# Optimization experiments

Hardware: AMD Instinct MI355X
Metric: run time of the kernel (lower is better)

Reference implementation:

```python
import jax, jax.numpy as jnp
import numpy as np

N_NODES = 100000
N_EDGES = 1600000
IN_CH = 128          # 127 node features + 1 node_attr
HIDDEN = 2           # hidd_FV_size
OUT_CH = 128
ATTR = 6


def setup_inputs() -> dict:
    key = jax.random.key(0)
    ks = jax.random.split(key, 8)
    x = jax.random.normal(ks[0], (N_NODES, IN_CH - 1), dtype=jnp.float32)
    node_attr = jax.random.normal(ks[1], (N_NODES, 1), dtype=jnp.float32)
    edge_index = jax.random.randint(ks[2], (2, N_EDGES), 0, N_NODES, dtype=jnp.int64)
    edge_attr = jax.random.normal(ks[3], (N_EDGES, ATTR), dtype=jnp.float32)
    # lin_in: Linear(ATTR, HIDDEN * IN_CH); lin_out: Linear(HIDDEN * IN_CH, OUT_CH)
    W_in = jax.random.normal(ks[4], (ATTR, HIDDEN * IN_CH), dtype=jnp.float32) / np.sqrt(ATTR)
    b_in = jax.random.normal(ks[5], (HIDDEN * IN_CH,), dtype=jnp.float32) * 0.01
    W_out = jax.random.normal(ks[6], (HIDDEN * IN_CH, OUT_CH), dtype=jnp.float32) / np.sqrt(HIDDEN * IN_CH)
    b_out = jax.random.normal(ks[7], (OUT_CH,), dtype=jnp.float32) * 0.01
    return {"x": x, "node_attr": node_attr, "edge_index": edge_index,
            "edge_attr": edge_attr, "W_in": W_in, "b_in": b_in,
            "W_out": W_out, "b_out": b_out}


def reference(x, node_attr, edge_index, edge_attr, W_in, b_in, W_out, b_out):
    # forward: x = cat(x, node_attr) -> propagate(aggr='add') -> update
    xc = jnp.concatenate([x, node_attr], axis=1)                # [N, IN_CH]
    src, dst = edge_index[0], edge_index[1]                     # PyG: message from x_j=src, aggregated at dst
    x_j = xc[src]                                               # [E, IN_CH] gather
    # message: scaling = relu(lin_in(edge_attr)); result = scaling.reshape(E,C,H) * x_j[...,None]
    scaling = jax.nn.relu(edge_attr @ W_in + b_in)              # [E, C*H]
    msg = (scaling.reshape(-1, IN_CH, HIDDEN) * x_j[:, :, None]).reshape(-1, IN_CH * HIDDEN)
    # aggregate: scatter-add over destination nodes
    aggr = jax.ops.segment_sum(msg, dst, num_segments=N_NODES)  # [N, C*H]
    # update: lin_out -> tanh (dropout p=0 / eval mode)
    return jnp.tanh(aggr @ W_out + b_out)                       # [N, OUT_CH]
```

## Files before the change

### kernel.cpp

```cpp
#include <hip/hip_runtime.h>


#define ATTR 6
#define SCAN_CHUNK 1024


__global__ __launch_bounds__(256) void hist_kernel(
    const int* __restrict__ ei, int* __restrict__ counts, int E)
{
  const int e0 = blockIdx.x * 1024 + threadIdx.x * 4;
  if (((E & 3) == 0) && (e0 + 4 <= E)) {
    const int4 d = *(const int4*)(ei + E + e0);
    atomicAdd(&counts[d.x], 1);
    atomicAdd(&counts[d.y], 1);
    atomicAdd(&counts[d.z], 1);
    atomicAdd(&counts[d.w], 1);
  } else {
#pragma unroll
    for (int j = 0; j < 4; ++j) {
      const int e = e0 + j;
      if (e < E) atomicAdd(&counts[ei[E + e]], 1);
    }
  }
}


__global__ __launch_bounds__(256) void scan1_kernel(
    const int* __restrict__ counts, int* __restrict__ offsets,
    int* __restrict__ bsum, int N)
{
  __shared__ int sdata[256];
  const int t = threadIdx.x;
  const int base = blockIdx.x * SCAN_CHUNK + t * 4;
  int c[4]; int s = 0;
#pragma unroll
  for (int j = 0; j < 4; ++j) { int i = base + j; c[j] = (i < N) ? counts[i] : 0; s += c[j]; }
  sdata[t] = s;
  __syncthreads();
  for (int d = 1; d < 256; d <<= 1) {
    int tv = (t >= d) ? sdata[t - d] : 0;
    __syncthreads();
    sdata[t] += tv;
    __syncthreads();
  }
  int excl = sdata[t] - s;
#pragma unroll
  for (int j = 0; j < 4; ++j) { int i = base + j; if (i < N) offsets[i] = excl; excl += c[j]; }
  if (t == 255) bsum[blockIdx.x] = sdata[255];
}


__global__ __launch_bounds__(256) void scanB_kernel(
    int* __restrict__ offsets, int* __restrict__ cursors,
    const int* __restrict__ bsum, int N, int E)
{
  __shared__ int red[4];
  const int t = threadIdx.x;
  int v = 0;
  for (int k = t; k < (int)blockIdx.x; k += 256) v += bsum[k];
#pragma unroll
  for (int d = 32; d > 0; d >>= 1) v += __shfl_down(v, d, 64);
  if ((t & 63) == 0) red[t >> 6] = v;
  __syncthreads();
  const int add = red[0] + red[1] + red[2] + red[3];

  const int base = blockIdx.x * SCAN_CHUNK + t * 4;
#pragma unroll
  for (int j = 0; j < 4; ++j) {
    const int i = base + j;
    if (i < N) { const int o = offsets[i] + add; offsets[i] = o; cursors[i] = o; }
  }
  if (blockIdx.x == 0 && t == 0) offsets[N] = E;
}


__global__ __launch_bounds__(256) void scatter_concat_kernel(
    const int* __restrict__ ei, const float* __restrict__ ea,
    int* __restrict__ cursors, int* __restrict__ srcs, float* __restrict__ eas,
    const float* __restrict__ x, const float* __restrict__ na,
    float* __restrict__ xc, int E, int N, int SB)
{
  if ((int)blockIdx.x < SB) {
    const int e = blockIdx.x * 256 + threadIdx.x;
    if (e < E) {
      const int dst = ei[E + e];
      const int slot = atomicAdd(&cursors[dst], 1);
      srcs[slot] = ei[e];
      const float2 a0 = *(const float2*)(ea + (size_t)e * ATTR + 0);
      const float2 a1 = *(const float2*)(ea + (size_t)e * ATTR + 2);
      const float2 a2 = *(const float2*)(ea + (size_t)e * ATTR + 4);
      float* ep = eas + (size_t)slot * ATTR;
      *(float2*)(ep + 0) = a0;
      *(float2*)(ep + 2) = a1;
      *(float2*)(ep + 4) = a2;
    }
  } else {
    const int gid = (blockIdx.x - SB) * 256 + threadIdx.x;
    const int row = gid >> 5;
    const int c4 = (gid & 31) * 4;
    if (row < N) {
      const float* xr = x + (size_t)row * 127;
      float4 v;
      v.x = xr[c4];
      v.y = xr[c4 + 1];
      v.z = xr[c4 + 2];
      v.w = (c4 == 124) ? na[row] : xr[c4 + 3];
      *(float4*)(xc + (size_t)row * 128 + c4) = v;
    }
  }
}


__global__ __launch_bounds__(256) void aggregate8b_kernel(
    const float* __restrict__ xc,
    const float* __restrict__ W_in, const float* __restrict__ b_in,
    const int* __restrict__ offsets, const int* __restrict__ srcs,
    const float* __restrict__ eas,
    float* __restrict__ aggr, int N)
{
  const int L = threadIdx.x & 63;
  const int n = __builtin_amdgcn_readfirstlane(blockIdx.x * 4 + (threadIdx.x >> 6));
  if (n >= N) return;

  float2 wlo[ATTR], whi[ATTR];
#pragma unroll
  for (int a = 0; a < ATTR; ++a) {
    wlo[a] = *(const float2*)(W_in + a * 256 + 2 * L);
    whi[a] = *(const float2*)(W_in + a * 256 + 128 + 2 * L);
  }
  const float2 blo = *(const float2*)(b_in + 2 * L);
  const float2 bhi = *(const float2*)(b_in + 128 + 2 * L);

  float alo0 = 0.f, alo1 = 0.f, ahi0 = 0.f, ahi1 = 0.f;
  const int beg = __builtin_amdgcn_readfirstlane(offsets[n]);
  const int end = __builtin_amdgcn_readfirstlane(offsets[n + 1]);

  int i0 = beg;
  for (; i0 + 8 <= end; i0 += 8) {
    int s8[8];
#pragma unroll
    for (int j = 0; j < 8; ++j) s8[j] = srcs[i0 + j];
    float eav[8][ATTR];
#pragma unroll
    for (int j = 0; j < 8; ++j)
#pragma unroll
      for (int a = 0; a < ATTR; ++a) eav[j][a] = eas[(size_t)(i0 + j) * ATTR + a];

    float xlo[8], xhi[8];
#pragma unroll
    for (int j = 0; j < 8; ++j) {
      const float* xr = xc + (size_t)s8[j] * 128;
      xlo[j] = xr[L];
      xhi[j] = xr[64 + L];
    }
#pragma unroll
    for (int j = 0; j < 8; ++j) {
      float sl0 = blo.x, sl1 = blo.y, sh0 = bhi.x, sh1 = bhi.y;
#pragma unroll
      for (int a = 0; a < ATTR; ++a) {
        sl0 = fmaf(eav[j][a], wlo[a].x, sl0);
        sl1 = fmaf(eav[j][a], wlo[a].y, sl1);
        sh0 = fmaf(eav[j][a], whi[a].x, sh0);
        sh1 = fmaf(eav[j][a], whi[a].y, sh1);
      }
      sl0 = fmaxf(sl0, 0.f); sl1 = fmaxf(sl1, 0.f);
      sh0 = fmaxf(sh0, 0.f); sh1 = fmaxf(sh1, 0.f);
      alo0 = fmaf(sl0, xlo[j], alo0);
      alo1 = fmaf(sl1, xlo[j], alo1);
      ahi0 = fmaf(sh0, xhi[j], ahi0);
      ahi1 = fmaf(sh1, xhi[j], ahi1);
    }
  }
  if (i0 + 4 <= end) {
    int s4[4];
#pragma unroll
    for (int j = 0; j < 4; ++j) s4[j] = srcs[i0 + j];
    float eav[4][ATTR];
#pragma unroll
    for (int j = 0; j < 4; ++j)
#pragma unroll
      for (int a = 0; a < ATTR; ++a) eav[j][a] = eas[(size_t)(i0 + j) * ATTR + a];
    float xlo[4], xhi[4];
#pragma unroll
    for (int j = 0; j < 4; ++j) {
      const float* xr = xc + (size_t)s4[j] * 128;
      xlo[j] = xr[L];
      xhi[j] = xr[64 + L];
    }
#pragma unroll
    for (int j = 0; j < 4; ++j) {
      float sl0 = blo.x, sl1 = blo.y, sh0 = bhi.x, sh1 = bhi.y;
#pragma unroll
      for (int a = 0; a < ATTR; ++a) {
        sl0 = fmaf(eav[j][a], wlo[a].x, sl0);
        sl1 = fmaf(eav[j][a], wlo[a].y, sl1);
        sh0 = fmaf(eav[j][a], whi[a].x, sh0);
        sh1 = fmaf(eav[j][a], whi[a].y, sh1);
      }
      sl0 = fmaxf(sl0, 0.f); sl1 = fmaxf(sl1, 0.f);
      sh0 = fmaxf(sh0, 0.f); sh1 = fmaxf(sh1, 0.f);
      alo0 = fmaf(sl0, xlo[j], alo0);
      alo1 = fmaf(sl1, xlo[j], alo1);
      ahi0 = fmaf(sh0, xhi[j], ahi0);
      ahi1 = fmaf(sh1, xhi[j], ahi1);
    }
    i0 += 4;
  }
  for (; i0 < end; ++i0) {
    const int s = srcs[i0];
    float eav[ATTR];
#pragma unroll
    for (int a = 0; a < ATTR; ++a) eav[a] = eas[(size_t)i0 * ATTR + a];
    const float* xr = xc + (size_t)s * 128;
    const float xl = xr[L];
    const float xh = xr[64 + L];
    float sl0 = blo.x, sl1 = blo.y, sh0 = bhi.x, sh1 = bhi.y;
#pragma unroll
    for (int a = 0; a < ATTR; ++a) {
      sl0 = fmaf(eav[a], wlo[a].x, sl0);
      sl1 = fmaf(eav[a], wlo[a].y, sl1);
      sh0 = fmaf(eav[a], whi[a].x, sh0);
      sh1 = fmaf(eav[a], whi[a].y, sh1);
    }
    sl0 = fmaxf(sl0, 0.f); sl1 = fmaxf(sl1, 0.f);
    sh0 = fmaxf(sh0, 0.f); sh1 = fmaxf(sh1, 0.f);
    alo0 = fmaf(sl0, xl, alo0);
    alo1 = fmaf(sl1, xl, alo1);
    ahi0 = fmaf(sh0, xh, ahi0);
    ahi1 = fmaf(sh1, xh, ahi1);
  }

  *(float2*)(aggr + (size_t)n * 256 + 2 * L)       = make_float2(alo0, alo1);
  *(float2*)(aggr + (size_t)n * 256 + 128 + 2 * L) = make_float2(ahi0, ahi1);
}


__global__ __launch_bounds__(256) void scatter_kernel(
    const int* __restrict__ ei, int* __restrict__ cursors,
    int* __restrict__ perm, int* __restrict__ srcs, int E)
{
  int e = blockIdx.x * 256 + threadIdx.x;
  if (e < E) {
    int dst = ei[E + e];
    int slot = atomicAdd(&cursors[dst], 1);
    perm[slot] = e;
    srcs[slot] = ei[e];
  }
}

__global__ __launch_bounds__(256) void aggregate4_kernel(
    const float* __restrict__ x, const float* __restrict__ node_attr,
    const int* __restrict__ ei, const float* __restrict__ ea,
    const float* __restrict__ W_in, const float* __restrict__ b_in,
    const int* __restrict__ offsets, const int* __restrict__ perm,
    const int* __restrict__ srcs,
    float* __restrict__ aggr, int N)
{
  const int L = threadIdx.x & 63;
  const int n = __builtin_amdgcn_readfirstlane(blockIdx.x * 4 + (threadIdx.x >> 6));
  if (n >= N) return;

  float2 wlo[ATTR], whi[ATTR];
#pragma unroll
  for (int a = 0; a < ATTR; ++a) {
    wlo[a] = *(const float2*)(W_in + a * 256 + 2 * L);
    whi[a] = *(const float2*)(W_in + a * 256 + 128 + 2 * L);
  }
  const float2 blo = *(const float2*)(b_in + 2 * L);
  const float2 bhi = *(const float2*)(b_in + 128 + 2 * L);

  float alo0 = 0.f, alo1 = 0.f, ahi0 = 0.f, ahi1 = 0.f;
  const int beg = offsets[n], end = offsets[n + 1];

  for (int i0 = beg; i0 < end; i0 += 4) {
    const int cnt = end - i0;
    int e4[4], s4[4];
#pragma unroll
    for (int j = 0; j < 4; ++j) {
      const int idx = i0 + ((j < cnt) ? j : cnt - 1);
      e4[j] = perm[idx];
      s4[j] = srcs[idx];
    }
    float eav[4][ATTR];
#pragma unroll
    for (int j = 0; j < 4; ++j)
#pragma unroll
      for (int a = 0; a < ATTR; ++a) eav[j][a] = ea[(size_t)e4[j] * ATTR + a];
    float xlo[4], xhi[4];
#pragma unroll
    for (int j = 0; j < 4; ++j) {
      const float* xr = x + (size_t)s4[j] * 127;
      xlo[j] = xr[L];
      xhi[j] = (L == 63) ? node_attr[s4[j]] : xr[64 + L];
    }
#pragma unroll
    for (int j = 0; j < 4; ++j)
      if (j >= cnt) { xlo[j] = 0.f; xhi[j] = 0.f; }
#pragma unroll
    for (int j = 0; j < 4; ++j) {
      float sl0 = blo.x, sl1 = blo.y, sh0 = bhi.x, sh1 = bhi.y;
#pragma unroll
      for (int a = 0; a < ATTR; ++a) {
        sl0 = fmaf(eav[j][a], wlo[a].x, sl0);
        sl1 = fmaf(eav[j][a], wlo[a].y, sl1);
        sh0 = fmaf(eav[j][a], whi[a].x, sh0);
        sh1 = fmaf(eav[j][a], whi[a].y, sh1);
      }
      sl0 = fmaxf(sl0, 0.f); sl1 = fmaxf(sl1, 0.f);
      sh0 = fmaxf(sh0, 0.f); sh1 = fmaxf(sh1, 0.f);
      alo0 = fmaf(sl0, xlo[j], alo0);
      alo1 = fmaf(sl1, xlo[j], alo1);
      ahi0 = fmaf(sh0, xhi[j], ahi0);
      ahi1 = fmaf(sh1, xhi[j], ahi1);
    }
  }

  *(float2*)(aggr + (size_t)n * 256 + 2 * L)       = make_float2(alo0, alo1);
  *(float2*)(aggr + (size_t)n * 256 + 128 + 2 * L) = make_float2(ahi0, ahi1);
}


__global__ __launch_bounds__(256) void edge_kernel(
    const float* __restrict__ x, const float* __restrict__ node_attr,
    const int* __restrict__ ei, const float* __restrict__ ea,
    const float* __restrict__ W_in, const float* __restrict__ b_in,
    float* __restrict__ aggr, int E, int N, int epw)
{
  const int lane = threadIdx.x & 63;
  const int wave = blockIdx.x * (blockDim.x >> 6) + (threadIdx.x >> 6);
  const int k0 = lane << 2;
  const int c0 = lane << 1;

  float w[ATTR][4];
#pragma unroll
  for (int a = 0; a < ATTR; ++a) {
    const float4 t = *(const float4*)(W_in + a * 256 + k0);
    w[a][0] = t.x; w[a][1] = t.y; w[a][2] = t.z; w[a][3] = t.w;
  }
  const float4 bt = *(const float4*)(b_in + k0);

  const long e0 = (long)wave * epw;
  for (int i = 0; i < epw; ++i) {
    const long e = e0 + i;
    if (e >= E) return;
    const int src = ei[e];
    const int dst = ei[E + e];

    float eav[ATTR];
#pragma unroll
    for (int a = 0; a < ATTR; ++a) eav[a] = ea[(size_t)e * ATTR + a];

    float s0 = bt.x, s1 = bt.y, s2 = bt.z, s3 = bt.w;
#pragma unroll
    for (int a = 0; a < ATTR; ++a) {
      s0 = fmaf(eav[a], w[a][0], s0);
      s1 = fmaf(eav[a], w[a][1], s1);
      s2 = fmaf(eav[a], w[a][2], s2);
      s3 = fmaf(eav[a], w[a][3], s3);
    }
    s0 = fmaxf(s0, 0.f); s1 = fmaxf(s1, 0.f);
    s2 = fmaxf(s2, 0.f); s3 = fmaxf(s3, 0.f);

    const float* xr = x + (size_t)src * 127;
    const float x0 = xr[c0];
    const float x1 = (lane == 63) ? node_attr[src] : xr[c0 + 1];

    float* ap = aggr + (size_t)dst * 256 + k0;
    atomicAdd(ap + 0, s0 * x0);
    atomicAdd(ap + 1, s1 * x0);
    atomicAdd(ap + 2, s2 * x1);
    atomicAdd(ap + 3, s3 * x1);
  }
}


__global__ __launch_bounds__(256) void node_kernel2(
    const float* __restrict__ aggr, const float* __restrict__ W_out,
    const float* __restrict__ b_out, float* __restrict__ out, int N)
{
  __shared__ float Wl[64 * 128];
  __shared__ float Al[64][68];
  const int t = threadIdx.x;
  const int o4 = (t & 31) * 4;
  const int ng = t >> 5;
  const int nbase = blockIdx.x * 64;

  float acc[8][4];
#pragma unroll
  for (int j = 0; j < 8; ++j)
#pragma unroll
    for (int q = 0; q < 4; ++q) acc[j][q] = 0.f;

  for (int kc = 0; kc < 4; ++kc) {
    __syncthreads();
    const float4* wsrc = (const float4*)(W_out + kc * 64 * 128);
    float4* wdst = (float4*)Wl;
#pragma unroll
    for (int i = 0; i < 8; ++i) wdst[t + 256 * i] = wsrc[t + 256 * i];
    {
      const int r = t >> 2, q = t & 3;
      int row = nbase + r; if (row >= N) row = N - 1;
      const float4* asrc = (const float4*)(aggr + (size_t)row * 256 + kc * 64 + q * 16);
      float4 v0 = asrc[0], v1 = asrc[1], v2 = asrc[2], v3 = asrc[3];
      float4* adst = (float4*)&Al[r][q * 16];
      adst[0] = v0; adst[1] = v1; adst[2] = v2; adst[3] = v3;
    }
    __syncthreads();

    for (int k = 0; k < 64; k += 4) {
      float4 a4[8];
#pragma unroll
      for (int j = 0; j < 8; ++j) a4[j] = *(const float4*)&Al[ng * 8 + j][k];
#pragma unroll
      for (int kk = 0; kk < 4; ++kk) {
        const float4 w4 = *(const float4*)&Wl[(k + kk) * 128 + o4];
#pragma unroll
        for (int j = 0; j < 8; ++j) {
          const float av = (&a4[j].x)[kk];
          acc[j][0] = fmaf(av, w4.x, acc[j][0]);
          acc[j][1] = fmaf(av, w4.y, acc[j][1]);
          acc[j][2] = fmaf(av, w4.z, acc[j][2]);
          acc[j][3] = fmaf(av, w4.w, acc[j][3]);
        }
      }
    }
  }

  const float4 b4 = *(const float4*)(b_out + o4);
#pragma unroll
  for (int j = 0; j < 8; ++j) {
    const int n = nbase + ng * 8 + j;
    if (n < N) {
      float4 r;
      r.x = tanhf(acc[j][0] + b4.x);
      r.y = tanhf(acc[j][1] + b4.y);
      r.z = tanhf(acc[j][2] + b4.z);
      r.w = tanhf(acc[j][3] + b4.w);
      *(float4*)(out + (size_t)n * 128 + o4) = r;
    }
  }
}


extern "C" void kernel_launch(void* const* d_in, const int* in_sizes, int n_in,
                              void* d_out, int out_size, void* d_ws, size_t ws_size,
                              hipStream_t stream) {
  const float* x         = (const float*)d_in[0];
  const float* node_attr = (const float*)d_in[1];
  const int*   ei        = (const int*)d_in[2];
  const float* ea        = (const float*)d_in[3];
  const float* W_in      = (const float*)d_in[4];
  const float* b_in      = (const float*)d_in[5];
  const float* W_out     = (const float*)d_in[6];
  const float* b_out     = (const float*)d_in[7];
  float* out = (float*)d_out;

  const int N = in_sizes[0] / 127;
  const int E = in_sizes[2] / 2;

  auto align16 = [](size_t v) { return (v + 15) & ~(size_t)15; };
  const size_t szCounts  = align16((size_t)N * 4);
  const size_t szOffsets = align16(((size_t)N + 1) * 4);
  const size_t szCursors = align16((size_t)N * 4);
  const size_t szBsum    = align16(((size_t)N / SCAN_CHUNK + 2) * 4);
  const size_t szPerm    = align16((size_t)E * 4);
  const size_t szSrcs    = align16((size_t)E * 4);
  const size_t szEas     = align16((size_t)E * ATTR * 4);
  const size_t szXc      = align16((size_t)N * 128 * 4);
  const size_t szAggr    = (size_t)N * 256 * 4;

  const size_t needA = szCounts + szOffsets + szCursors + szBsum +
                       szSrcs + szEas + szXc + szAggr;
  const size_t needB = szCounts + szOffsets + szCursors + szBsum +
                       szPerm + szSrcs + szAggr;

  const int nodeBlocks = (N + 63) / 64;
  const int histBlocks = (E + 1023) / 1024;
  const int nb = (N + SCAN_CHUNK - 1) / SCAN_CHUNK;
  const int SB = (E + 255) / 256;
  const int CB = (N * 32 + 255) / 256;

  if (ws_size >= needA) {
    char* p = (char*)d_ws;
    int* counts   = (int*)p;     p += szCounts;
    int* offsets  = (int*)p;     p += szOffsets;
    int* cursors  = (int*)p;     p += szCursors;
    int* bsum     = (int*)p;     p += szBsum;
    int* srcs     = (int*)p;     p += szSrcs;
    float* eas    = (float*)p;   p += szEas;
    float* xc     = (float*)p;   p += szXc;
    float* aggr   = (float*)p;

    hipMemsetAsync(counts, 0, szCounts, stream);
    hist_kernel<<<histBlocks, 256, 0, stream>>>(ei, counts, E);
    scan1_kernel<<<nb, 256, 0, stream>>>(counts, offsets, bsum, N);
    scanB_kernel<<<nb, 256, 0, stream>>>(offsets, cursors, bsum, N, E);
    scatter_concat_kernel<<<SB + CB, 256, 0, stream>>>(
        ei, ea, cursors, srcs, eas, x, node_attr, xc, E, N, SB);
    aggregate8b_kernel<<<(N + 3) / 4, 256, 0, stream>>>(
        xc, W_in, b_in, offsets, srcs, eas, aggr, N);
    node_kernel2<<<nodeBlocks, 256, 0, stream>>>(aggr, W_out, b_out, out, N);
  } else if (ws_size >= needB) {
    char* p = (char*)d_ws;
    int* counts   = (int*)p;     p += szCounts;
    int* offsets  = (int*)p;     p += szOffsets;
    int* cursors  = (int*)p;     p += szCursors;
    int* bsum     = (int*)p;     p += szBsum;
    int* perm     = (int*)p;     p += szPerm;
    int* srcs     = (int*)p;     p += szSrcs;
    float* aggr   = (float*)p;

    hipMemsetAsync(counts, 0, szCounts, stream);
    hist_kernel<<<histBlocks, 256, 0, stream>>>(ei, counts, E);
    scan1_kernel<<<nb, 256, 0, stream>>>(counts, offsets, bsum, N);
    scanB_kernel<<<nb, 256, 0, stream>>>(offsets, cursors, bsum, N, E);
    scatter_kernel<<<SB, 256, 0, stream>>>(ei, cursors, perm, srcs, E);
    aggregate4_kernel<<<(N + 3) / 4, 256, 0, stream>>>(
        x, node_attr, ei, ea, W_in, b_in, offsets, perm, srcs, aggr, N);
    node_kernel2<<<nodeBlocks, 256, 0, stream>>>(aggr, W_out, b_out, out, N);
  } else {
    float* aggr = (float*)d_ws;
    hipMemsetAsync(aggr, 0, (size_t)N * 256 * 4, stream);
    const int EPW = 4;
    const int waves = (E + EPW - 1) / EPW;
    edge_kernel<<<(waves + 3) / 4, 256, 0, stream>>>(
        x, node_attr, ei, ea, W_in, b_in, aggr, E, N, EPW);
    node_kernel2<<<nodeBlocks, 256, 0, stream>>>(aggr, W_out, b_out, out, N);
  }
}
```

Before: 565.4 us.

## Pack CSR edge payload into 32-byte records and use packed float2 FMA

The scatter stage now writes the source index and six edge attributes into one 32-byte record per sorted slot, instead of separate srcs and eas arrays. The new aggregation kernel reads each record as two float4 loads, gathers a float2 per lane from the concatenated node features, and computes scaling and accumulation with float2 FMA helpers that could map to packed FP32 instructions. The output GEMM kernel is also rewritten with float2 accumulators, and 64-bit index math is replaced with 32-bit. The packed layout uses a little more workspace because of the padding slot, and 32-bit indexing limits the maximum problem size.

```diff
diff --git a/kernel.cpp b/kernel.cpp
--- a/kernel.cpp
+++ b/kernel.cpp
@@ -3,6 +3,15 @@
 
 #define ATTR 6
 #define SCAN_CHUNK 1024
+
+
+__device__ __forceinline__ float2 f2fma(float2 a, float2 b, float2 c) {
+  return make_float2(fmaf(a.x, b.x, c.x), fmaf(a.y, b.y, c.y));
+}
+__device__ __forceinline__ float2 f2max0(float2 a) {
+  return make_float2(fmaxf(a.x, 0.f), fmaxf(a.y, 0.f));
+}
+__device__ __forceinline__ float2 f2splat(float x) { return make_float2(x, x); }
 
 
 __global__ __launch_bounds__(256) void hist_kernel(
@@ -71,6 +80,111 @@
     if (i < N) { const int o = offsets[i] + add; offsets[i] = o; cursors[i] = o; }
   }
   if (blockIdx.x == 0 && t == 0) offsets[N] = E;
+}
+
+
+__global__ __launch_bounds__(256) void scatter_concat2_kernel(
+    const int* __restrict__ ei, const float* __restrict__ ea,
+    int* __restrict__ cursors, float* __restrict__ pay,
+    const float* __restrict__ x, const float* __restrict__ na,
+    float* __restrict__ xc, int E, int N, int SB)
+{
+  if ((int)blockIdx.x < SB) {
+    const int e = blockIdx.x * 256 + threadIdx.x;
+    if (e < E) {
+      const int dst = ei[E + e];
+      const int slot = atomicAdd(&cursors[dst], 1);
+      const float2 a0 = *(const float2*)(ea + e * ATTR + 0);
+      const float2 a1 = *(const float2*)(ea + e * ATTR + 2);
+      const float2 a2 = *(const float2*)(ea + e * ATTR + 4);
+      float4* pp = (float4*)pay + 2 * slot;
+      pp[0] = make_float4(__int_as_float(ei[e]), a0.x, a0.y, a1.x);
+      pp[1] = make_float4(a1.y, a2.x, a2.y, 0.f);
+    }
+  } else {
+    const int gid = (blockIdx.x - SB) * 256 + threadIdx.x;
+    const int row = gid >> 5;
+    const int c4 = (gid & 31) * 4;
+    if (row < N) {
+      const float* xr = x + row * 127;
+      float4 v;
+      v.x = xr[c4];
+      v.y = xr[c4 + 1];
+      v.z = xr[c4 + 2];
+      v.w = (c4 == 124) ? na[row] : xr[c4 + 3];
+      *(float4*)(xc + row * 128 + c4) = v;
+    }
+  }
+}
+
+
+template <int G>
+__device__ __forceinline__ void agg_group(
+    const float4* pp, const float* xc, int L,
+    const float2* wA, const float2* wB, float2 bA, float2 bB,
+    float2& accA, float2& accB)
+{
+  float4 p0[G], p1[G];
+#pragma unroll
+  for (int j = 0; j < G; ++j) { p0[j] = pp[2 * j]; p1[j] = pp[2 * j + 1]; }
+  float2 xv[G];
+#pragma unroll
+  for (int j = 0; j < G; ++j) {
+    const int s = __float_as_int(p0[j].x);
+    xv[j] = *(const float2*)(xc + s * 128 + 2 * L);
+  }
+#pragma unroll
+  for (int j = 0; j < G; ++j) {
+    float2 sA = bA, sB = bB;
+    sA = f2fma(f2splat(p0[j].y), wA[0], sA); sB = f2fma(f2splat(p0[j].y), wB[0], sB);
+    sA = f2fma(f2splat(p0[j].z), wA[1], sA); sB = f2fma(f2splat(p0[j].z), wB[1], sB);
+    sA = f2fma(f2splat(p0[j].w), wA[2], sA); sB = f2fma(f2splat(p0[j].w), wB[2], sB);
+    sA = f2fma(f2splat(p1[j].x), wA[3], sA); sB = f2fma(f2splat(p1[j].x), wB[3], sB);
+    sA = f2fma(f2splat(p1[j].y), wA[4], sA); sB = f2fma(f2splat(p1[j].y), wB[4], sB);
+    sA = f2fma(f2splat(p1[j].z), wA[5], sA); sB = f2fma(f2splat(p1[j].z), wB[5], sB);
+    sA = f2max0(sA); sB = f2max0(sB);
+    accA = f2fma(f2splat(xv[j].x), sA, accA);
+    accB = f2fma(f2splat(xv[j].y), sB, accB);
+  }
+}
+
+__global__ __launch_bounds__(256) void aggregate_v3_kernel(
+    const float* __restrict__ xc,
+    const float* __restrict__ W_in, const float* __restrict__ b_in,
+    const int* __restrict__ offsets, const float* __restrict__ pay,
+    float* __restrict__ aggr, int N)
+{
+  const int L = (int)threadIdx.x & 63;
+  const int n = __builtin_amdgcn_readfirstlane((int)blockIdx.x * 4 + ((int)threadIdx.x >> 6));
+  if (n >= N) return;
+
+  float2 wA[ATTR], wB[ATTR];
+#pragma unroll
+  for (int a = 0; a < ATTR; ++a) {
+    const float4 w4 = *(const float4*)(W_in + a * 256 + 4 * L);
+    wA[a] = make_float2(w4.x, w4.y);
+    wB[a] = make_float2(w4.z, w4.w);
+  }
+  const float4 b4 = *(const float4*)(b_in + 4 * L);
+  const float2 bA = make_float2(b4.x, b4.y);
+  const float2 bB = make_float2(b4.z, b4.w);
+
+  float2 accA = make_float2(0.f, 0.f);
+  float2 accB = make_float2(0.f, 0.f);
+  const int beg = __builtin_amdgcn_readfirstlane(offsets[n]);
+  const int end = __builtin_amdgcn_readfirstlane(offsets[n + 1]);
+
+  int i0 = beg;
+  for (; i0 + 8 <= end; i0 += 8)
+    agg_group<8>((const float4*)pay + 2 * i0, xc, L, wA, wB, bA, bB, accA, accB);
+  if (i0 + 4 <= end) {
+    agg_group<4>((const float4*)pay + 2 * i0, xc, L, wA, wB, bA, bB, accA, accB);
+    i0 += 4;
+  }
+  for (; i0 < end; ++i0)
+    agg_group<1>((const float4*)pay + 2 * i0, xc, L, wA, wB, bA, bB, accA, accB);
+
+  *(float4*)(aggr + n * 256 + 4 * L) = make_float4(accA.x, accA.y, accB.x, accB.y);
 }
 
 
@@ -110,7 +224,6 @@
   }
 }
 
-
 __global__ __launch_bounds__(256) void aggregate8b_kernel(
     const float* __restrict__ xc,
     const float* __restrict__ W_in, const float* __restrict__ b_in,
@@ -374,7 +487,7 @@
 }
 
 
-__global__ __launch_bounds__(256) void node_kernel2(
+__global__ __launch_bounds__(256) void node_kernel3(
     const float* __restrict__ aggr, const float* __restrict__ W_out,
     const float* __restrict__ b_out, float* __restrict__ out, int N)
 {
@@ -385,11 +498,12 @@
   const int ng = t >> 5;
   const int nbase = blockIdx.x * 64;
 
-  float acc[8][4];
-#pragma unroll
-  for (int j = 0; j < 8; ++j)
-#pragma unroll
-    for (int q = 0; q < 4; ++q) acc[j][q] = 0.f;
+  float2 acc[8][2];
+#pragma unroll
+  for (int j = 0; j < 8; ++j) {
+    acc[j][0] = make_float2(0.f, 0.f);
+    acc[j][1] = make_float2(0.f, 0.f);
+  }
 
   for (int kc = 0; kc < 4; ++kc) {
     __syncthreads();
@@ -400,7 +514,7 @@
     {
       const int r = t >> 2, q = t & 3;
       int row = nbase + r; if (row >= N) row = N - 1;
-      const float4* asrc = (const float4*)(aggr + (size_t)row * 256 + kc * 64 + q * 16);
+      const float4* asrc = (const float4*)(aggr + row * 256 + kc * 64 + q * 16);
       float4 v0 = asrc[0], v1 = asrc[1], v2 = asrc[2], v3 = asrc[3];
       float4* adst = (float4*)&Al[r][q * 16];
       adst[0] = v0; adst[1] = v1; adst[2] = v2; adst[3] = v3;
@@ -414,13 +528,13 @@
 #pragma unroll
       for (int kk = 0; kk < 4; ++kk) {
         const float4 w4 = *(const float4*)&Wl[(k + kk) * 128 + o4];
+        const float2 wA = make_float2(w4.x, w4.y);
+        const float2 wB = make_float2(w4.z, w4.w);
 #pragma unroll
         for (int j = 0; j < 8; ++j) {
-          const float av = (&a4[j].x)[kk];
-          acc[j][0] = fmaf(av, w4.x, acc[j][0]);
-          acc[j][1] = fmaf(av, w4.y, acc[j][1]);
-          acc[j][2] = fmaf(av, w4.z, acc[j][2]);
-          acc[j][3] = fmaf(av, w4.w, acc[j][3]);
+          const float2 av = f2splat((&a4[j].x)[kk]);
+          acc[j][0] = f2fma(av, wA, acc[j][0]);
+          acc[j][1] = f2fma(av, wB, acc[j][1]);
         }
       }
     }
@@ -432,11 +546,11 @@
     const int n = nbase + ng * 8 + j;
     if (n < N) {
       float4 r;
-      r.x = tanhf(acc[j][0] + b4.x);
-      r.y = tanhf(acc[j][1] + b4.y);
-      r.z = tanhf(acc[j][2] + b4.z);
-      r.w = tanhf(acc[j][3] + b4.w);
-      *(float4*)(out + (size_t)n * 128 + o4) = r;
+      r.x = tanhf(acc[j][0].x + b4.x);
+      r.y = tanhf(acc[j][0].y + b4.y);
+      r.z = tanhf(acc[j][1].x + b4.z);
+      r.w = tanhf(acc[j][1].y + b4.w);
+      *(float4*)(out + n * 128 + o4) = r;
     }
   }
 }
@@ -466,13 +580,16 @@
   const size_t szPerm    = align16((size_t)E * 4);
   const size_t szSrcs    = align16((size_t)E * 4);
   const size_t szEas     = align16((size_t)E * ATTR * 4);
+  const size_t szPay     = align16((size_t)E * 8 * 4);
   const size_t szXc      = align16((size_t)N * 128 * 4);
   const size_t szAggr    = (size_t)N * 256 * 4;
 
-  const size_t needA = szCounts + szOffsets + szCursors + szBsum +
-                       szSrcs + szEas + szXc + szAggr;
-  const size_t needB = szCounts + szOffsets + szCursors + szBsum +
-                       szPerm + szSrcs + szAggr;
+  const size_t needA2 = szCounts + szOffsets + szCursors + szBsum +
+                        szPay + szXc + szAggr;
+  const size_t needA  = szCounts + szOffsets + szCursors + szBsum +
+                        szSrcs + szEas + szXc + szAggr;
+  const size_t needB  = szCounts + szOffsets + szCursors + szBsum +
+                        szPerm + szSrcs + szAggr;
 
   const int nodeBlocks = (N + 63) / 64;
   const int histBlocks = (E + 1023) / 1024;
@@ -480,7 +597,26 @@
   const int SB = (E + 255) / 256;
   const int CB = (N * 32 + 255) / 256;
 
-  if (ws_size >= needA) {
+  if (ws_size >= needA2) {
+    char* p = (char*)d_ws;
+    int* counts   = (int*)p;     p += szCounts;
+    int* offsets  = (int*)p;     p += szOffsets;
+    int* cursors  = (int*)p;     p += szCursors;
+    int* bsum     = (int*)p;     p += szBsum;
+    float* pay    = (float*)p;   p += szPay;
+    float* xc     = (float*)p;   p += szXc;
+    float* aggr   = (float*)p;
+
+    hipMemsetAsync(counts, 0, szCounts, stream);
+    hist_kernel<<<histBlocks, 256, 0, stream>>>(ei, counts, E);
+    scan1_kernel<<<nb, 256, 0, stream>>>(counts, offsets, bsum, N);
+    scanB_kernel<<<nb, 256, 0, stream>>>(offsets, cursors, bsum, N, E);
+    scatter_concat2_kernel<<<SB + CB, 256, 0, stream>>>(
+        ei, ea, cursors, pay, x, node_attr, xc, E, N, SB);
+    aggregate_v3_kernel<<<(N + 3) / 4, 256, 0, stream>>>(
+        xc, W_in, b_in, offsets, pay, aggr, N);
+    node_kernel3<<<nodeBlocks, 256, 0, stream>>>(aggr, W_out, b_out, out, N);
+  } else if (ws_size >= needA) {
     char* p = (char*)d_ws;
     int* counts   = (int*)p;     p += szCounts;
     int* offsets  = (int*)p;     p += szOffsets;
@@ -499,7 +635,7 @@
         ei, ea, cursors, srcs, eas, x, node_attr, xc, E, N, SB);
     aggregate8b_kernel<<<(N + 3) / 4, 256, 0, stream>>>(
         xc, W_in, b_in, offsets, srcs, eas, aggr, N);
-    node_kernel2<<<nodeBlocks, 256, 0, stream>>>(aggr, W_out, b_out, out, N);
+    node_kernel3<<<nodeBlocks, 256, 0, stream>>>(aggr, W_out, b_out, out, N);
   } else if (ws_size >= needB) {
     char* p = (char*)d_ws;
     int* counts   = (int*)p;     p += szCounts;
@@ -517,7 +653,7 @@
     scatter_kernel<<<SB, 256, 0, stream>>>(ei, cursors, perm, srcs, E);
     aggregate4_kernel<<<(N + 3) / 4, 256, 0, stream>>>(
         x, node_attr, ei, ea, W_in, b_in, offsets, perm, srcs, aggr, N);
-    node_kernel2<<<nodeBlocks, 256, 0, stream>>>(aggr, W_out, b_out, out, N);
+    node_kernel3<<<nodeBlocks, 256, 0, stream>>>(aggr, W_out, b_out, out, N);
   } else {
     float* aggr = (float*)d_ws;
     hipMemsetAsync(aggr, 0, (size_t)N * 256 * 4, stream);
@@ -525,6 +661,6 @@
     const int waves = (E + EPW - 1) / EPW;
     edge_kernel<<<(waves + 3) / 4, 256, 0, stream>>>(
         x, node_attr, ei, ea, W_in, b_in, aggr, E, N, EPW);
-    node_kernel2<<<nodeBlocks, 256, 0, stream>>>(aggr, W_out, b_out, out, N);
-  }
-}
+    node_kernel3<<<nodeBlocks, 256, 0, stream>>>(aggr, W_out, b_out, out, N);
+  }
+}
```

After: 550.5 us. 2.6% less time.
